# Kernel tuning notes

Hardware: AMD Instinct MI355X
Metric: run time of the kernel (lower is better)

## Reference

```python
import jax, jax.numpy as jnp
from jax import lax
import numpy as np

L = 8            # NMF rank (n_components)
NMF_ITERS = 50   # fixed multiplicative-update iterations
EPS = 1.1920929e-07  # float32 machine eps, as sklearn uses


def nmf_mu(V, key):
    """Multiplicative-update NMF (Frobenius loss), sklearn-style random init.
    V: [T, M] nonnegative. Returns W:[T,L], H:[L,M]."""
    T, M = V.shape
    kW, kH = jax.random.split(key)
    avg = jnp.sqrt(jnp.mean(V) / L)
    W0 = avg * jax.random.uniform(kW, (T, L), dtype=V.dtype)
    H0 = avg * jax.random.uniform(kH, (L, M), dtype=V.dtype)

    def step(carry, _):
        W, H = carry
        # H update: H *= (W^T V) / (W^T W H)
        H = H * (W.T @ V) / (W.T @ W @ H + EPS)
        # W update: W *= (V H^T) / (W H H^T)
        W = W * (V @ H.T) / (W @ (H @ H.T) + EPS)
        return (W, H), None

    (W, H), _ = lax.scan(step, (W0, H0), None, length=NMF_ITERS)
    return W, H


def pointwise_conv(w, x):
    # 1x1x1 Conv3d == channel mix: w [C_out, C_in], x [n, C_in, D, H, W]
    return jnp.einsum('oc,ncdhw->nodhw', w, x)


def setup_inputs() -> dict:
    key = jax.random.key(0)
    k0, k1, k2, k3, k4 = jax.random.split(key, 5)
    C = 64
    eps = jax.random.normal(k0, (1, C, 16, 64, 64), dtype=jnp.float32)
    s = 1.0 / np.sqrt(C)  # keep pre-activation variance ~1 (like torch init scale)
    w_pre = jax.random.normal(k1, (C, C), dtype=jnp.float32) * s
    b_pre = jax.random.normal(k2, (C,), dtype=jnp.float32) * s
    w_post1 = jax.random.normal(k3, (C, C), dtype=jnp.float32) * s
    w_post2 = jax.random.normal(k4, (C, C), dtype=jnp.float32) * s
    return {"eps": eps, "w_pre": w_pre, "b_pre": b_pre,
            "w_post1": w_post1, "w_post2": w_post2}


def reference(eps, w_pre, b_pre, w_post1, w_post2):
    n, t, k, a, b = eps.shape
    # xi_pre: 1x1x1 conv + bias + ReLU (ReLU guarantees nonnegative NMF input)
    Vst = jax.nn.relu(pointwise_conv(w_pre, eps) + b_pre[None, :, None, None, None])
    V = Vst.reshape(t, k * a * b)  # n == 1
    W, H = nmf_mu(V, jax.random.key(0))
    Vst_hat = (W @ H).reshape(n, t, k, a, b)
    error = jnp.linalg.norm(Vst - Vst_hat)  # torch.dist (Frobenius)
    # xi_post: conv(no bias) -> ReLU -> conv(no bias)
    y = jax.nn.relu(pointwise_conv(w_post1, Vst_hat))
    eps_hat = pointwise_conv(w_post2, y)
    return eps_hat, error
```

## Files before the change

### kernel.cpp

```cpp
#include <hip/hip_runtime.h>
#include <stdint.h>

#define JAX_PARTITIONABLE 1

constexpr int kC = 64;
constexpr int kS = 65536;
constexpr int kL = 8;
constexpr int kIters = 50;
constexpr int kBlocks = 256;
constexpr int kThreads = 512;
constexpr int kCols = 256;
constexpr int kGroups = 16;
constexpr int kEntries = 576;
constexpr float kEps = 1.1920929e-07f;

#define AGENT __HIP_MEMORY_SCOPE_AGENT

struct Ctl {
  unsigned root;  unsigned pad0[31];
  unsigned leaf[16][32];
  float mean_sum; float err_sum; float pad1[30];
  float B[3][kGroups][kEntries];
};

__device__ __forceinline__ uint2 tf2x32(unsigned k0, unsigned k1,
                                        unsigned x0, unsigned x1) {
  unsigned k2 = k0 ^ k1 ^ 0x1BD11BDAu;
  x0 += k0; x1 += k1;
#define TF_RND(r) { x0 += x1; x1 = (x1 << (r)) | (x1 >> (32 - (r))); x1 ^= x0; }
  TF_RND(13) TF_RND(15) TF_RND(26) TF_RND(6)
  x0 += k1; x1 += k2 + 1u;
  TF_RND(17) TF_RND(29) TF_RND(16) TF_RND(24)
  x0 += k2; x1 += k0 + 2u;
  TF_RND(13) TF_RND(15) TF_RND(26) TF_RND(6)
  x0 += k0; x1 += k1 + 3u;
  TF_RND(17) TF_RND(29) TF_RND(16) TF_RND(24)
  x0 += k1; x1 += k2 + 4u;
  TF_RND(13) TF_RND(15) TF_RND(26) TF_RND(6)
  x0 += k2; x1 += k0 + 5u;
#undef TF_RND
  return make_uint2(x0, x1);
}

__device__ __forceinline__ float u01(unsigned b) {
  return __uint_as_float((b >> 9) | 0x3f800000u) - 1.0f;
}

__device__ __forceinline__ void gridbar(Ctl* ctl, unsigned& round) {
  ++round;
  __syncthreads();
  if (threadIdx.x == 0) {
    const unsigned target = round * 16u;
    const unsigned leaf = blockIdx.x & 15u;
    unsigned a = __hip_atomic_fetch_add(&ctl->leaf[leaf][0], 1u,
                                        __ATOMIC_RELAXED, AGENT);
    if (a == target - 1u)
      __hip_atomic_fetch_add(&ctl->root, 1u, __ATOMIC_RELAXED, AGENT);
    while (__hip_atomic_load(&ctl->root, __ATOMIC_RELAXED, AGENT) < target)
      __builtin_amdgcn_s_sleep(1);
    __builtin_amdgcn_fence(__ATOMIC_ACQUIRE, "agent");
  }
  __syncthreads();
}

__global__ void init_ctl(unsigned* ws) {
  const unsigned n = (unsigned)(sizeof(Ctl) / 4);
  for (unsigned i = blockIdx.x * blockDim.x + threadIdx.x; i < n;
       i += gridDim.x * blockDim.x)
    ws[i] = 0u;
}

__global__ __launch_bounds__(kThreads, 2) void fsam_nmf(
    const float* __restrict__ eps, const float* __restrict__ w_pre,
    const float* __restrict__ b_pre, const float* __restrict__ w_post1,
    const float* __restrict__ w_post2, float* __restrict__ out, Ctl* ctl) {
  __shared__ __align__(16) float Vs[kC][260];
  __shared__ __align__(16) float Hs[kL][260];
  __shared__ __align__(16) float Pn[kL][260];
  __shared__ __align__(16) float Pv[4][512];
  __shared__ __align__(16) float Ph[16][64];
  __shared__ __align__(16) float Ws[kC][kL];
  __shared__ __align__(16) float WtWs[kL * kL];
  __shared__ __align__(16) float hhts[kL * kL];
  __shared__ float reds[8];

  const int tid = threadIdx.x;
  const int t = tid & 255;
  const int q = tid >> 8;
  const int obase = q * 32;
  const int s = blockIdx.x * kCols + t;
  unsigned bar_round = 0;

  float acc[32];
#pragma unroll
  for (int o = 0; o < 32; ++o) acc[o] = b_pre[obase + o];
  for (int c = 0; c < kC; ++c) {
    const float e = eps[c * kS + s];
#pragma unroll
    for (int o = 0; o < 32; ++o)
      acc[o] = fmaf(w_pre[(obase + o) * kC + c], e, acc[o]);
  }
  float lsum = 0.0f;
#pragma unroll
  for (int o = 0; o < 32; ++o) {
    acc[o] = fmaxf(acc[o], 0.0f);
    Vs[obase + o][t] = acc[o];
    lsum += acc[o];
  }
  {
    float r = lsum;
#pragma unroll
    for (int off = 32; off > 0; off >>= 1) r += __shfl_down(r, off, 64);
    if ((tid & 63) == 0) reds[tid >> 6] = r;
    __syncthreads();
    if (tid == 0) {
      float sm = 0.0f;
#pragma unroll
      for (int w = 0; w < 8; ++w) sm += reds[w];
      __hip_atomic_fetch_add(&ctl->mean_sum, sm, __ATOMIC_RELAXED, AGENT);
    }
  }
  gridbar(ctl, bar_round);
  const float avg = sqrtf(
      __hip_atomic_load(&ctl->mean_sum, __ATOMIC_RELAXED, AGENT) *
      (1.0f / (4194304.0f * 8.0f)));

#if JAX_PARTITIONABLE
  const uint2 kw = tf2x32(0u, 0u, 0u, 0u);
  const uint2 kh = tf2x32(0u, 0u, 0u, 1u);
#else
  const uint2 A0 = tf2x32(0u, 0u, 0u, 2u);
  const uint2 A1 = tf2x32(0u, 0u, 1u, 3u);
  const uint2 kw = make_uint2(A0.x, A1.x);
  const uint2 kh = make_uint2(A0.y, A1.y);
#endif

  float h[kL] = {0, 0, 0, 0, 0, 0, 0, 0};
  if (q == 0) {
#if JAX_PARTITIONABLE
#pragma unroll
    for (int l = 0; l < kL; ++l) {
      uint2 r = tf2x32(kh.x, kh.y, 0u, (unsigned)(l * kS + s));
      h[l] = avg * u01(r.x ^ r.y);
    }
#else
#pragma unroll
    for (int l = 0; l < 4; ++l) {
      unsigned i = (unsigned)(l * kS + s);
      uint2 r = tf2x32(kh.x, kh.y, i, i + 262144u);
      h[l] = avg * u01(r.x);
      h[l + 4] = avg * u01(r.y);
    }
#endif
  }
  {
#if JAX_PARTITIONABLE
    uint2 r0 = tf2x32(kw.x, kw.y, 0u, (unsigned)tid);
    (&Ws[0][0])[tid] = avg * u01(r0.x ^ r0.y);
#else
    if (tid < 256) {
      uint2 r = tf2x32(kw.x, kw.y, (unsigned)tid, (unsigned)(tid + 256));
      (&Ws[0][0])[tid] = avg * u01(r.x);
      (&Ws[0][0])[tid + 256] = avg * u01(r.y);
    }
#endif
  }
  __syncthreads();
  if (tid < kL * kL) {
    const int l = tid >> 3, j = tid & 7;
    float sum = 0.0f;
    for (int c = 0; c < kC; ++c) sum = fmaf(Ws[c][l], Ws[c][j], sum);
    WtWs[tid] = sum;
  }
  __syncthreads();

  for (int it = 0; it < kIters; ++it) {
    float num[kL] = {0, 0, 0, 0, 0, 0, 0, 0};
    for (int ci = 0; ci < 32; ++ci) {
      const int c = obase + ci;
      const float v = Vs[c][t];
      const float4 w0 = *(const float4*)&Ws[c][0];
      const float4 w1 = *(const float4*)&Ws[c][4];
      num[0] = fmaf(v, w0.x, num[0]); num[1] = fmaf(v, w0.y, num[1]);
      num[2] = fmaf(v, w0.z, num[2]); num[3] = fmaf(v, w0.w, num[3]);
      num[4] = fmaf(v, w1.x, num[4]); num[5] = fmaf(v, w1.y, num[5]);
      num[6] = fmaf(v, w1.z, num[6]); num[7] = fmaf(v, w1.w, num[7]);
    }
    if (q == 1) {
#pragma unroll
      for (int l = 0; l < kL; ++l) Pn[l][t] = num[l];
    }
    __syncthreads();
    if (q == 0) {
      float hn[kL];
#pragma unroll
      for (int l = 0; l < kL; ++l) {
        const float4 a = *(const float4*)&WtWs[l * kL];
        const float4 b = *(const float4*)&WtWs[l * kL + 4];
        float d = kEps;
        d = fmaf(a.x, h[0], d); d = fmaf(a.y, h[1], d);
        d = fmaf(a.z, h[2], d); d = fmaf(a.w, h[3], d);
        d = fmaf(b.x, h[4], d); d = fmaf(b.y, h[5], d);
        d = fmaf(b.z, h[6], d); d = fmaf(b.w, h[7], d);
        hn[l] = h[l] * (num[l] + Pn[l][t]) / d;
      }
#pragma unroll
      for (int l = 0; l < kL; ++l) { h[l] = hn[l]; Hs[l][t] = hn[l]; }
    } else if ((blockIdx.x >> 4) == 1) {
      float* nb = &ctl->B[(it + 1) % 3][blockIdx.x & 15][0];
      for (int k = t; k < kEntries; k += 256)
        __hip_atomic_store(&nb[k], 0.0f, __ATOMIC_RELAXED, AGENT);
    }
    __syncthreads();

    {
      const int range = tid >> 7;
      const int tile = tid & 127;
      const int c0 = (tile >> 2) * 2;
      const int l0 = (tile & 3) * 2;
      const int sbeg = range * 64;
      float a00 = 0, a01 = 0, a10 = 0, a11 = 0;
      for (int s4 = sbeg; s4 < sbeg + 64; s4 += 4) {
        const float4 h0 = *(const float4*)&Hs[l0][s4];
        const float4 h1 = *(const float4*)&Hs[l0 + 1][s4];
        const float4 v0 = *(const float4*)&Vs[c0][s4];
        const float4 v1 = *(const float4*)&Vs[c0 + 1][s4];
        a00 = fmaf(v0.x, h0.x, a00); a00 = fmaf(v0.y, h0.y, a00);
        a00 = fmaf(v0.z, h0.z, a00); a00 = fmaf(v0.w, h0.w, a00);
        a01 = fmaf(v0.x, h1.x, a01); a01 = fmaf(v0.y, h1.y, a01);
        a01 = fmaf(v0.z, h1.z, a01); a01 = fmaf(v0.w, h1.w, a01);
        a10 = fmaf(v1.x, h0.x, a10); a10 = fmaf(v1.y, h0.y, a10);
        a10 = fmaf(v1.z, h0.z, a10); a10 = fmaf(v1.w, h0.w, a10);
        a11 = fmaf(v1.x, h1.x, a11); a11 = fmaf(v1.y, h1.y, a11);
        a11 = fmaf(v1.z, h1.z, a11); a11 = fmaf(v1.w, h1.w, a11);
      }
      Pv[range][c0 * 8 + l0] = a00;
      Pv[range][c0 * 8 + l0 + 1] = a01;
      Pv[range][(c0 + 1) * 8 + l0] = a10;
      Pv[range][(c0 + 1) * 8 + l0 + 1] = a11;
    }
    if (tid < 256) {
      const int tile = tid >> 4, range = tid & 15;
      const int j0 = (tile >> 2) * 2, l0 = (tile & 3) * 2;
      const int sbeg = range * 16;
      float a00 = 0, a01 = 0, a10 = 0, a11 = 0;
      for (int s4 = sbeg; s4 < sbeg + 16; s4 += 4) {
        const float4 x0 = *(const float4*)&Hs[j0][s4];
        const float4 x1 = *(const float4*)&Hs[j0 + 1][s4];
        const float4 y0 = *(const float4*)&Hs[l0][s4];
        const float4 y1 = *(const float4*)&Hs[l0 + 1][s4];
        a00 = fmaf(x0.x, y0.x, a00); a00 = fmaf(x0.y, y0.y, a00);
        a00 = fmaf(x0.z, y0.z, a00); a00 = fmaf(x0.w, y0.w, a00);
        a01 = fmaf(x0.x, y1.x, a01); a01 = fmaf(x0.y, y1.y, a01);
        a01 = fmaf(x0.z, y1.z, a01); a01 = fmaf(x0.w, y1.w, a01);
        a10 = fmaf(x1.x, y0.x, a10); a10 = fmaf(x1.y, y0.y, a10);
        a10 = fmaf(x1.z, y0.z, a10); a10 = fmaf(x1.w, y0.w, a10);
        a11 = fmaf(x1.x, y1.x, a11); a11 = fmaf(x1.y, y1.y, a11);
        a11 = fmaf(x1.z, y1.z, a11); a11 = fmaf(x1.w, y1.w, a11);
      }
      Ph[range][j0 * 8 + l0] = a00;
      Ph[range][j0 * 8 + l0 + 1] = a01;
      Ph[range][(j0 + 1) * 8 + l0] = a10;
      Ph[range][(j0 + 1) * 8 + l0 + 1] = a11;
    }
    __syncthreads();

    float* Bg = &ctl->B[it % 3][blockIdx.x & 15][0];
    {
      const float v = Pv[0][tid & 511] + Pv[1][tid & 511] +
                      Pv[2][tid & 511] + Pv[3][tid & 511];
      __hip_atomic_fetch_add(&Bg[tid], v, __ATOMIC_RELAXED, AGENT);
    }
    if (tid >= 448) {
      const int e = tid - 448;
      float v = 0.0f;
#pragma unroll
      for (int r = 0; r < 16; ++r) v += Ph[r][e];
      __hip_atomic_fetch_add(&Bg[512 + e], v, __ATOMIC_RELAXED, AGENT);
    }

    gridbar(ctl, bar_round);

    const float* Bb = &ctl->B[it % 3][0][0];
    float v = 0.0f;
    {
#pragma unroll
      for (int g = 0; g < kGroups; ++g) v += Bb[g * kEntries + tid];
    }
    if (tid < kL * kL) {
      float sum = 0.0f;
#pragma unroll
      for (int g = 0; g < kGroups; ++g) sum += Bb[g * kEntries + 512 + tid];
      hhts[tid] = sum;
    }
    __syncthreads();
    float wn;
    {
      const int c0 = tid >> 3, l0 = tid & 7;
      float d = kEps;
#pragma unroll
      for (int j = 0; j < kL; ++j) d = fmaf(Ws[c0][j], hhts[j * kL + l0], d);
      wn = (&Ws[0][0])[tid] * v / d;
    }
    __syncthreads();
    (&Ws[0][0])[tid] = wn;
    __syncthreads();
    if (tid < kL * kL) {
      const int l = tid >> 3, j = tid & 7;
      float sum = 0.0f;
      for (int c = 0; c < kC; ++c) sum = fmaf(Ws[c][l], Ws[c][j], sum);
      WtWs[tid] = sum;
    }
    __syncthreads();
  }

  if (q == 1) {
#pragma unroll
    for (int l = 0; l < kL; ++l) h[l] = Hs[l][t];
  }
  float errp = 0.0f;
  for (int ci = 0; ci < 32; ++ci) {
    const int c = obase + ci;
    const float4 w0 = *(const float4*)&Ws[c][0];
    const float4 w1 = *(const float4*)&Ws[c][4];
    float tcc = 0.0f;
    tcc = fmaf(w0.x, h[0], tcc); tcc = fmaf(w0.y, h[1], tcc);
    tcc = fmaf(w0.z, h[2], tcc); tcc = fmaf(w0.w, h[3], tcc);
    tcc = fmaf(w1.x, h[4], tcc); tcc = fmaf(w1.y, h[5], tcc);
    tcc = fmaf(w1.z, h[6], tcc); tcc = fmaf(w1.w, h[7], tcc);
    const float d = Vs[c][t] - tcc;
    errp = fmaf(d, d, errp);
    Vs[c][t] = tcc;
  }
  {
    float r = errp;
#pragma unroll
    for (int off = 32; off > 0; off >>= 1) r += __shfl_down(r, off, 64);
    __syncthreads();
    if ((tid & 63) == 0) reds[tid >> 6] = r;
    __syncthreads();
    if (tid == 0) {
      float sm = 0.0f;
#pragma unroll
      for (int w = 0; w < 8; ++w) sm += reds[w];
      __hip_atomic_fetch_add(&ctl->err_sum, sm, __ATOMIC_RELAXED, AGENT);
    }
  }
  __syncthreads();
  float yacc[32];
#pragma unroll
  for (int o = 0; o < 32; ++o) yacc[o] = 0.0f;
  for (int c = 0; c < kC; ++c) {
    const float vv = Vs[c][t];
#pragma unroll
    for (int o = 0; o < 32; ++o)
      yacc[o] = fmaf(w_post1[(obase + o) * kC + c], vv, yacc[o]);
  }
  __syncthreads();
#pragma unroll
  for (int o = 0; o < 32; ++o) Vs[obase + o][t] = fmaxf(yacc[o], 0.0f);
  __syncthreads();
  float outacc[32];
#pragma unroll
  for (int o = 0; o < 32; ++o) outacc[o] = 0.0f;
  for (int c = 0; c < kC; ++c) {
    const float yv = Vs[c][t];
#pragma unroll
    for (int o = 0; o < 32; ++o)
      outacc[o] = fmaf(w_post2[(obase + o) * kC + c], yv, outacc[o]);
  }
#pragma unroll
  for (int o = 0; o < 32; ++o) out[(obase + o) * kS + s] = outacc[o];

  gridbar(ctl, bar_round);
  if (blockIdx.x == 0 && tid == 0)
    out[kC * kS] = sqrtf(__hip_atomic_load(&ctl->err_sum, __ATOMIC_RELAXED, AGENT));
}

extern "C" void kernel_launch(void* const* d_in, const int* in_sizes, int n_in,
                              void* d_out, int out_size, void* d_ws, size_t ws_size,
                              hipStream_t stream) {
  (void)in_sizes; (void)n_in; (void)out_size; (void)ws_size;
  const float* eps     = (const float*)d_in[0];
  const float* w_pre   = (const float*)d_in[1];
  const float* b_pre   = (const float*)d_in[2];
  const float* w_post1 = (const float*)d_in[3];
  const float* w_post2 = (const float*)d_in[4];
  float* out = (float*)d_out;
  Ctl* ctl = (Ctl*)d_ws;

  init_ctl<<<64, 256, 0, stream>>>((unsigned*)d_ws);
  fsam_nmf<<<kBlocks, kThreads, 0, stream>>>(eps, w_pre, b_pre, w_post1,
                                             w_post2, out, ctl);
}
```

Before: 741.3 us.

## Restructure NMF kernel with transposed V tile, register-resident V, fewer reduction groups

Reworks the per-block NMF loop. V now lives in registers as two columns per thread, with a transposed shared-memory copy used for the V·H^T reduction. The numerator partial sums are split across four channel groups, and W^T W is computed in parallel chunks inside the loop instead of by 64 threads serially. The number of global reduction groups drops from 16 to 4. The goal is to cut shared-memory traffic and serial per-iteration work, at the cost of more atomic contention per group and more register pressure.

```diff
diff --git a/kernel.cpp b/kernel.cpp
--- a/kernel.cpp
+++ b/kernel.cpp
@@ -10,8 +10,11 @@
 constexpr int kBlocks = 256;
 constexpr int kThreads = 512;
 constexpr int kCols = 256;
-constexpr int kGroups = 16;
+constexpr int kGroups = 4;
 constexpr int kEntries = 576;
+constexpr int kHP = 260;
+constexpr int kVP = 68;
+constexpr int kNP = 258;
 constexpr float kEps = 1.1920929e-07f;
 
 #define AGENT __HIP_MEMORY_SCOPE_AGENT
@@ -50,12 +53,12 @@
   ++round;
   __syncthreads();
   if (threadIdx.x == 0) {
-    const unsigned target = round * 16u;
     const unsigned leaf = blockIdx.x & 15u;
     unsigned a = __hip_atomic_fetch_add(&ctl->leaf[leaf][0], 1u,
                                         __ATOMIC_RELAXED, AGENT);
-    if (a == target - 1u)
+    if (a == round * 16u - 1u)
       __hip_atomic_fetch_add(&ctl->root, 1u, __ATOMIC_RELAXED, AGENT);
+    const unsigned target = round * 16u;
     while (__hip_atomic_load(&ctl->root, __ATOMIC_RELAXED, AGENT) < target)
       __builtin_amdgcn_s_sleep(1);
     __builtin_amdgcn_fence(__ATOMIC_ACQUIRE, "agent");
@@ -74,38 +77,49 @@
     const float* __restrict__ eps, const float* __restrict__ w_pre,
     const float* __restrict__ b_pre, const float* __restrict__ w_post1,
     const float* __restrict__ w_post2, float* __restrict__ out, Ctl* ctl) {
-  __shared__ __align__(16) float Vs[kC][260];
-  __shared__ __align__(16) float Hs[kL][260];
-  __shared__ __align__(16) float Pn[kL][260];
-  __shared__ __align__(16) float Pv[4][512];
+  __shared__ __align__(16) float Vt[kCols][kVP];
+  __shared__ __align__(16) float Hs[kL][kHP];
+  __shared__ __align__(16) float Pn[4][kL][kNP];
+  __shared__ __align__(16) float Pv[8][512];
   __shared__ __align__(16) float Ph[16][64];
+  __shared__ __align__(16) float Pw[8][64];
   __shared__ __align__(16) float Ws[kC][kL];
-  __shared__ __align__(16) float WtWs[kL * kL];
-  __shared__ __align__(16) float hhts[kL * kL];
+  __shared__ __align__(16) float WtWs[64];
+  __shared__ __align__(16) float hhts[64];
   __shared__ float reds[8];
 
   const int tid = threadIdx.x;
-  const int t = tid & 255;
-  const int q = tid >> 8;
-  const int obase = q * 32;
-  const int s = blockIdx.x * kCols + t;
+  const int g = tid >> 7;
+  const int p = tid & 127;
+  const int obase = g * 16;
+  const int sb = blockIdx.x * kCols;
   unsigned bar_round = 0;
 
-  float acc[32];
-#pragma unroll
-  for (int o = 0; o < 32; ++o) acc[o] = b_pre[obase + o];
+  float vreg[2][16];
+#pragma unroll
+  for (int o = 0; o < 16; ++o) { vreg[0][o] = b_pre[obase + o]; vreg[1][o] = vreg[0][o]; }
   for (int c = 0; c < kC; ++c) {
-    const float e = eps[c * kS + s];
-#pragma unroll
-    for (int o = 0; o < 32; ++o)
-      acc[o] = fmaf(w_pre[(obase + o) * kC + c], e, acc[o]);
+    const float2 e2 = *(const float2*)(eps + (size_t)c * kS + sb + 2 * p);
+#pragma unroll
+    for (int o = 0; o < 16; ++o) {
+      const float w = w_pre[(obase + o) * kC + c];
+      vreg[0][o] = fmaf(w, e2.x, vreg[0][o]);
+      vreg[1][o] = fmaf(w, e2.y, vreg[1][o]);
+    }
   }
   float lsum = 0.0f;
 #pragma unroll
-  for (int o = 0; o < 32; ++o) {
-    acc[o] = fmaxf(acc[o], 0.0f);
-    Vs[obase + o][t] = acc[o];
-    lsum += acc[o];
+  for (int col = 0; col < 2; ++col) {
+#pragma unroll
+    for (int o = 0; o < 16; ++o) {
+      vreg[col][o] = fmaxf(vreg[col][o], 0.0f);
+      lsum += vreg[col][o];
+    }
+#pragma unroll
+    for (int k = 0; k < 4; ++k)
+      *(float4*)&Vt[2 * p + col][obase + 4 * k] =
+          make_float4(vreg[col][4 * k], vreg[col][4 * k + 1],
+                      vreg[col][4 * k + 2], vreg[col][4 * k + 3]);
   }
   {
     float r = lsum;
@@ -134,22 +148,21 @@
   const uint2 kw = make_uint2(A0.x, A1.x);
   const uint2 kh = make_uint2(A0.y, A1.y);
 #endif
-
-  float h[kL] = {0, 0, 0, 0, 0, 0, 0, 0};
-  if (q == 0) {
+  if (tid < 256) {
+    const int s = sb + tid;
 #if JAX_PARTITIONABLE
 #pragma unroll
     for (int l = 0; l < kL; ++l) {
       uint2 r = tf2x32(kh.x, kh.y, 0u, (unsigned)(l * kS + s));
-      h[l] = avg * u01(r.x ^ r.y);
+      Hs[l][tid] = avg * u01(r.x ^ r.y);
     }
 #else
 #pragma unroll
     for (int l = 0; l < 4; ++l) {
       unsigned i = (unsigned)(l * kS + s);
       uint2 r = tf2x32(kh.x, kh.y, i, i + 262144u);
-      h[l] = avg * u01(r.x);
-      h[l + 4] = avg * u01(r.y);
+      Hs[l][tid] = avg * u01(r.x);
+      Hs[l + 4][tid] = avg * u01(r.y);
     }
 #endif
   }
@@ -166,85 +179,74 @@
 #endif
   }
   __syncthreads();
-  if (tid < kL * kL) {
-    const int l = tid >> 3, j = tid & 7;
-    float sum = 0.0f;
-    for (int c = 0; c < kC; ++c) sum = fmaf(Ws[c][l], Ws[c][j], sum);
-    WtWs[tid] = sum;
-  }
-  __syncthreads();
 
   for (int it = 0; it < kIters; ++it) {
-    float num[kL] = {0, 0, 0, 0, 0, 0, 0, 0};
-    for (int ci = 0; ci < 32; ++ci) {
-      const int c = obase + ci;
-      const float v = Vs[c][t];
-      const float4 w0 = *(const float4*)&Ws[c][0];
-      const float4 w1 = *(const float4*)&Ws[c][4];
-      num[0] = fmaf(v, w0.x, num[0]); num[1] = fmaf(v, w0.y, num[1]);
-      num[2] = fmaf(v, w0.z, num[2]); num[3] = fmaf(v, w0.w, num[3]);
-      num[4] = fmaf(v, w1.x, num[4]); num[5] = fmaf(v, w1.y, num[5]);
-      num[6] = fmaf(v, w1.z, num[6]); num[7] = fmaf(v, w1.w, num[7]);
-    }
-    if (q == 1) {
-#pragma unroll
-      for (int l = 0; l < kL; ++l) Pn[l][t] = num[l];
-    }
-    __syncthreads();
-    if (q == 0) {
-      float hn[kL];
-#pragma unroll
-      for (int l = 0; l < kL; ++l) {
-        const float4 a = *(const float4*)&WtWs[l * kL];
-        const float4 b = *(const float4*)&WtWs[l * kL + 4];
-        float d = kEps;
-        d = fmaf(a.x, h[0], d); d = fmaf(a.y, h[1], d);
-        d = fmaf(a.z, h[2], d); d = fmaf(a.w, h[3], d);
-        d = fmaf(b.x, h[4], d); d = fmaf(b.y, h[5], d);
-        d = fmaf(b.z, h[6], d); d = fmaf(b.w, h[7], d);
-        hn[l] = h[l] * (num[l] + Pn[l][t]) / d;
+    {
+      const int e = tid & 63, chunk = tid >> 6, cb = chunk * 8;
+      const int l = e >> 3, j = e & 7;
+      float s = 0.0f;
+#pragma unroll
+      for (int cc = 0; cc < 8; ++cc)
+        s = fmaf(Ws[cb + cc][l], Ws[cb + cc][j], s);
+      Pw[chunk][e] = s;
+    }
+    {
+      float num[2][kL] = {};
+#pragma unroll
+      for (int ci = 0; ci < 16; ++ci) {
+        const int c = obase + ci;
+        const float4 w0 = *(const float4*)&Ws[c][0];
+        const float4 w1 = *(const float4*)&Ws[c][4];
+        const float v0 = vreg[0][ci], v1 = vreg[1][ci];
+        num[0][0] = fmaf(v0, w0.x, num[0][0]); num[0][1] = fmaf(v0, w0.y, num[0][1]);
+        num[0][2] = fmaf(v0, w0.z, num[0][2]); num[0][3] = fmaf(v0, w0.w, num[0][3]);
+        num[0][4] = fmaf(v0, w1.x, num[0][4]); num[0][5] = fmaf(v0, w1.y, num[0][5]);
+        num[0][6] = fmaf(v0, w1.z, num[0][6]); num[0][7] = fmaf(v0, w1.w, num[0][7]);
+        num[1][0] = fmaf(v1, w0.x, num[1][0]); num[1][1] = fmaf(v1, w0.y, num[1][1]);
+        num[1][2] = fmaf(v1, w0.z, num[1][2]); num[1][3] = fmaf(v1, w0.w, num[1][3]);
+        num[1][4] = fmaf(v1, w1.x, num[1][4]); num[1][5] = fmaf(v1, w1.y, num[1][5]);
+        num[1][6] = fmaf(v1, w1.z, num[1][6]); num[1][7] = fmaf(v1, w1.w, num[1][7]);
       }
 #pragma unroll
-      for (int l = 0; l < kL; ++l) { h[l] = hn[l]; Hs[l][t] = hn[l]; }
-    } else if ((blockIdx.x >> 4) == 1) {
-      float* nb = &ctl->B[(it + 1) % 3][blockIdx.x & 15][0];
-      for (int k = t; k < kEntries; k += 256)
-        __hip_atomic_store(&nb[k], 0.0f, __ATOMIC_RELAXED, AGENT);
-    }
-    __syncthreads();
-
-    {
-      const int range = tid >> 7;
-      const int tile = tid & 127;
-      const int c0 = (tile >> 2) * 2;
-      const int l0 = (tile & 3) * 2;
-      const int sbeg = range * 64;
+      for (int l = 0; l < kL; ++l)
+        *(float2*)&Pn[g][l][2 * p] = make_float2(num[0][l], num[1][l]);
+    }
+    __syncthreads();
+    const int col = tid & 255, lh = tid >> 8;
+    float h[kL], nm[4];
+#pragma unroll
+    for (int l = 0; l < kL; ++l) h[l] = Hs[l][col];
+#pragma unroll
+    for (int k = 0; k < 4; ++k) {
+      const int l = lh * 4 + k;
+      nm[k] = Pn[0][l][col] + Pn[1][l][col] + Pn[2][l][col] + Pn[3][l][col];
+    }
+    if (tid < 64) {
+      float s = 0.0f;
+#pragma unroll
+      for (int r = 0; r < 8; ++r) s += Pw[r][tid];
+      WtWs[tid] = s;
+    }
+    __syncthreads();
+#pragma unroll
+    for (int k = 0; k < 4; ++k) {
+      const int l = lh * 4 + k;
+      const float4 a = *(const float4*)&WtWs[l * kL];
+      const float4 b = *(const float4*)&WtWs[l * kL + 4];
+      float d = kEps;
+      d = fmaf(a.x, h[0], d); d = fmaf(a.y, h[1], d);
+      d = fmaf(a.z, h[2], d); d = fmaf(a.w, h[3], d);
+      d = fmaf(b.x, h[4], d); d = fmaf(b.y, h[5], d);
+      d = fmaf(b.z, h[6], d); d = fmaf(b.w, h[7], d);
+      Hs[l][col] = h[l] * nm[k] / d;
+    }
+    __syncthreads();
+    if (tid < 256) {
+      const int tle = tid & 15, rng = tid >> 4;
+      const int j0 = (tle >> 2) * 2, l0 = (tle & 3) * 2;
+      const int s0 = rng * 16;
       float a00 = 0, a01 = 0, a10 = 0, a11 = 0;
-      for (int s4 = sbeg; s4 < sbeg + 64; s4 += 4) {
-        const float4 h0 = *(const float4*)&Hs[l0][s4];
-        const float4 h1 = *(const float4*)&Hs[l0 + 1][s4];
-        const float4 v0 = *(const float4*)&Vs[c0][s4];
-        const float4 v1 = *(const float4*)&Vs[c0 + 1][s4];
-        a00 = fmaf(v0.x, h0.x, a00); a00 = fmaf(v0.y, h0.y, a00);
-        a00 = fmaf(v0.z, h0.z, a00); a00 = fmaf(v0.w, h0.w, a00);
-        a01 = fmaf(v0.x, h1.x, a01); a01 = fmaf(v0.y, h1.y, a01);
-        a01 = fmaf(v0.z, h1.z, a01); a01 = fmaf(v0.w, h1.w, a01);
-        a10 = fmaf(v1.x, h0.x, a10); a10 = fmaf(v1.y, h0.y, a10);
-        a10 = fmaf(v1.z, h0.z, a10); a10 = fmaf(v1.w, h0.w, a10);
-        a11 = fmaf(v1.x, h1.x, a11); a11 = fmaf(v1.y, h1.y, a11);
-        a11 = fmaf(v1.z, h1.z, a11); a11 = fmaf(v1.w, h1.w, a11);
-      }
-      Pv[range][c0 * 8 + l0] = a00;
-      Pv[range][c0 * 8 + l0 + 1] = a01;
-      Pv[range][(c0 + 1) * 8 + l0] = a10;
-      Pv[range][(c0 + 1) * 8 + l0 + 1] = a11;
-    }
-    if (tid < 256) {
-      const int tile = tid >> 4, range = tid & 15;
-      const int j0 = (tile >> 2) * 2, l0 = (tile & 3) * 2;
-      const int sbeg = range * 16;
-      float a00 = 0, a01 = 0, a10 = 0, a11 = 0;
-      for (int s4 = sbeg; s4 < sbeg + 16; s4 += 4) {
+      for (int s4 = s0; s4 < s0 + 16; s4 += 4) {
         const float4 x0 = *(const float4*)&Hs[j0][s4];
         const float4 x1 = *(const float4*)&Hs[j0 + 1][s4];
         const float4 y0 = *(const float4*)&Hs[l0][s4];
@@ -258,80 +260,127 @@
         a11 = fmaf(x1.x, y1.x, a11); a11 = fmaf(x1.y, y1.y, a11);
         a11 = fmaf(x1.z, y1.z, a11); a11 = fmaf(x1.w, y1.w, a11);
       }
-      Ph[range][j0 * 8 + l0] = a00;
-      Ph[range][j0 * 8 + l0 + 1] = a01;
-      Ph[range][(j0 + 1) * 8 + l0] = a10;
-      Ph[range][(j0 + 1) * 8 + l0 + 1] = a11;
-    }
-    __syncthreads();
-
-    float* Bg = &ctl->B[it % 3][blockIdx.x & 15][0];
+      Ph[rng][j0 * 8 + l0] = a00;
+      Ph[rng][j0 * 8 + l0 + 1] = a01;
+      Ph[rng][(j0 + 1) * 8 + l0] = a10;
+      Ph[rng][(j0 + 1) * 8 + l0 + 1] = a11;
+    }
     {
-      const float v = Pv[0][tid & 511] + Pv[1][tid & 511] +
-                      Pv[2][tid & 511] + Pv[3][tid & 511];
+      const int tile = tid & 63, rng = tid >> 6;
+      const int cq = tile & 15, lp = tile >> 4;
+      const int cb = cq * 4, lb = lp * 2;
+      float acc[4][2] = {};
+      for (int s4 = rng * 32; s4 < rng * 32 + 32; s4 += 4) {
+        const float4 h0 = *(const float4*)&Hs[lb][s4];
+        const float4 h1 = *(const float4*)&Hs[lb + 1][s4];
+        const float4 va = *(const float4*)&Vt[s4][cb];
+        const float4 vb = *(const float4*)&Vt[s4 + 1][cb];
+        const float4 vc = *(const float4*)&Vt[s4 + 2][cb];
+        const float4 vd = *(const float4*)&Vt[s4 + 3][cb];
+        acc[0][0] = fmaf(va.x, h0.x, acc[0][0]); acc[0][1] = fmaf(va.x, h1.x, acc[0][1]);
+        acc[1][0] = fmaf(va.y, h0.x, acc[1][0]); acc[1][1] = fmaf(va.y, h1.x, acc[1][1]);
+        acc[2][0] = fmaf(va.z, h0.x, acc[2][0]); acc[2][1] = fmaf(va.z, h1.x, acc[2][1]);
+        acc[3][0] = fmaf(va.w, h0.x, acc[3][0]); acc[3][1] = fmaf(va.w, h1.x, acc[3][1]);
+        acc[0][0] = fmaf(vb.x, h0.y, acc[0][0]); acc[0][1] = fmaf(vb.x, h1.y, acc[0][1]);
+        acc[1][0] = fmaf(vb.y, h0.y, acc[1][0]); acc[1][1] = fmaf(vb.y, h1.y, acc[1][1]);
+        acc[2][0] = fmaf(vb.z, h0.y, acc[2][0]); acc[2][1] = fmaf(vb.z, h1.y, acc[2][1]);
+        acc[3][0] = fmaf(vb.w, h0.y, acc[3][0]); acc[3][1] = fmaf(vb.w, h1.y, acc[3][1]);
+        acc[0][0] = fmaf(vc.x, h0.z, acc[0][0]); acc[0][1] = fmaf(vc.x, h1.z, acc[0][1]);
+        acc[1][0] = fmaf(vc.y, h0.z, acc[1][0]); acc[1][1] = fmaf(vc.y, h1.z, acc[1][1]);
+        acc[2][0] = fmaf(vc.z, h0.z, acc[2][0]); acc[2][1] = fmaf(vc.z, h1.z, acc[2][1]);
+        acc[3][0] = fmaf(vc.w, h0.z, acc[3][0]); acc[3][1] = fmaf(vc.w, h1.z, acc[3][1]);
+        acc[0][0] = fmaf(vd.x, h0.w, acc[0][0]); acc[0][1] = fmaf(vd.x, h1.w, acc[0][1]);
+        acc[1][0] = fmaf(vd.y, h0.w, acc[1][0]); acc[1][1] = fmaf(vd.y, h1.w, acc[1][1]);
+        acc[2][0] = fmaf(vd.z, h0.w, acc[2][0]); acc[2][1] = fmaf(vd.z, h1.w, acc[2][1]);
+        acc[3][0] = fmaf(vd.w, h0.w, acc[3][0]); acc[3][1] = fmaf(vd.w, h1.w, acc[3][1]);
+      }
+#pragma unroll
+      for (int j = 0; j < 4; ++j)
+        *(float2*)&Pv[rng][cq * 32 + lp * 8 + j * 2] =
+            make_float2(acc[j][0], acc[j][1]);
+    }
+    __syncthreads();
+    float* Bg = &ctl->B[it % 3][blockIdx.x & 3][0];
+    {
+      const int c = tid >> 3, l = tid & 7;
+      const int slot = (c >> 2) * 32 + (l >> 1) * 8 + (c & 3) * 2 + (l & 1);
+      float v = 0.0f;
+#pragma unroll
+      for (int r = 0; r < 8; ++r) v += Pv[r][slot];
       __hip_atomic_fetch_add(&Bg[tid], v, __ATOMIC_RELAXED, AGENT);
     }
-    if (tid >= 448) {
-      const int e = tid - 448;
+    if (tid < 64) {
       float v = 0.0f;
 #pragma unroll
-      for (int r = 0; r < 16; ++r) v += Ph[r][e];
-      __hip_atomic_fetch_add(&Bg[512 + e], v, __ATOMIC_RELAXED, AGENT);
+      for (int r = 0; r < 16; ++r) v += Ph[r][tid];
+      __hip_atomic_fetch_add(&Bg[512 + tid], v, __ATOMIC_RELAXED, AGENT);
+    }
+    if ((blockIdx.x >> 2) == 4) {
+      float* nb = &ctl->B[(it + 1) % 3][blockIdx.x & 3][0];
+      __hip_atomic_store(&nb[tid], 0.0f, __ATOMIC_RELAXED, AGENT);
+      if (tid < 64)
+        __hip_atomic_store(&nb[512 + tid], 0.0f, __ATOMIC_RELAXED, AGENT);
     }
 
     gridbar(ctl, bar_round);
 
     const float* Bb = &ctl->B[it % 3][0][0];
-    float v = 0.0f;
-    {
-#pragma unroll
-      for (int g = 0; g < kGroups; ++g) v += Bb[g * kEntries + tid];
-    }
-    if (tid < kL * kL) {
-      float sum = 0.0f;
-#pragma unroll
-      for (int g = 0; g < kGroups; ++g) sum += Bb[g * kEntries + 512 + tid];
-      hhts[tid] = sum;
+    float v = Bb[tid] + Bb[kEntries + tid] + Bb[2 * kEntries + tid] +
+              Bb[3 * kEntries + tid];
+    if (tid < 64) {
+      hhts[tid] = Bb[512 + tid] + Bb[kEntries + 512 + tid] +
+                  Bb[2 * kEntries + 512 + tid] + Bb[3 * kEntries + 512 + tid];
     }
     __syncthreads();
     float wn;
     {
       const int c0 = tid >> 3, l0 = tid & 7;
+      const float4 w0 = *(const float4*)&Ws[c0][0];
+      const float4 w1 = *(const float4*)&Ws[c0][4];
       float d = kEps;
-#pragma unroll
-      for (int j = 0; j < kL; ++j) d = fmaf(Ws[c0][j], hhts[j * kL + l0], d);
+      d = fmaf(w0.x, hhts[l0], d);      d = fmaf(w0.y, hhts[8 + l0], d);
+      d = fmaf(w0.z, hhts[16 + l0], d); d = fmaf(w0.w, hhts[24 + l0], d);
+      d = fmaf(w1.x, hhts[32 + l0], d); d = fmaf(w1.y, hhts[40 + l0], d);
+      d = fmaf(w1.z, hhts[48 + l0], d); d = fmaf(w1.w, hhts[56 + l0], d);
       wn = (&Ws[0][0])[tid] * v / d;
     }
     __syncthreads();
     (&Ws[0][0])[tid] = wn;
     __syncthreads();
-    if (tid < kL * kL) {
-      const int l = tid >> 3, j = tid & 7;
-      float sum = 0.0f;
-      for (int c = 0; c < kC; ++c) sum = fmaf(Ws[c][l], Ws[c][j], sum);
-      WtWs[tid] = sum;
-    }
-    __syncthreads();
-  }
-
-  if (q == 1) {
-#pragma unroll
-    for (int l = 0; l < kL; ++l) h[l] = Hs[l][t];
+  }
+
+  float h2[2][kL];
+#pragma unroll
+  for (int l = 0; l < kL; ++l) {
+    const float2 t2 = *(const float2*)&Hs[l][2 * p];
+    h2[0][l] = t2.x; h2[1][l] = t2.y;
   }
   float errp = 0.0f;
-  for (int ci = 0; ci < 32; ++ci) {
+  float vh[2][16];
+#pragma unroll
+  for (int ci = 0; ci < 16; ++ci) {
     const int c = obase + ci;
     const float4 w0 = *(const float4*)&Ws[c][0];
     const float4 w1 = *(const float4*)&Ws[c][4];
-    float tcc = 0.0f;
-    tcc = fmaf(w0.x, h[0], tcc); tcc = fmaf(w0.y, h[1], tcc);
-    tcc = fmaf(w0.z, h[2], tcc); tcc = fmaf(w0.w, h[3], tcc);
-    tcc = fmaf(w1.x, h[4], tcc); tcc = fmaf(w1.y, h[5], tcc);
-    tcc = fmaf(w1.z, h[6], tcc); tcc = fmaf(w1.w, h[7], tcc);
-    const float d = Vs[c][t] - tcc;
-    errp = fmaf(d, d, errp);
-    Vs[c][t] = tcc;
-  }
+#pragma unroll
+    for (int colx = 0; colx < 2; ++colx) {
+      float t = 0.0f;
+      t = fmaf(w0.x, h2[colx][0], t); t = fmaf(w0.y, h2[colx][1], t);
+      t = fmaf(w0.z, h2[colx][2], t); t = fmaf(w0.w, h2[colx][3], t);
+      t = fmaf(w1.x, h2[colx][4], t); t = fmaf(w1.y, h2[colx][5], t);
+      t = fmaf(w1.z, h2[colx][6], t); t = fmaf(w1.w, h2[colx][7], t);
+      vh[colx][ci] = t;
+      const float d = vreg[colx][ci] - t;
+      errp = fmaf(d, d, errp);
+    }
+  }
+#pragma unroll
+  for (int colx = 0; colx < 2; ++colx)
+#pragma unroll
+    for (int k = 0; k < 4; ++k)
+      *(float4*)&Vt[2 * p + colx][obase + 4 * k] =
+          make_float4(vh[colx][4 * k], vh[colx][4 * k + 1],
+                      vh[colx][4 * k + 2], vh[colx][4 * k + 3]);
   {
     float r = errp;
 #pragma unroll
@@ -347,34 +396,50 @@
     }
   }
   __syncthreads();
-  float yacc[32];
-#pragma unroll
-  for (int o = 0; o < 32; ++o) yacc[o] = 0.0f;
-  for (int c = 0; c < kC; ++c) {
-    const float vv = Vs[c][t];
-#pragma unroll
-    for (int o = 0; o < 32; ++o)
-      yacc[o] = fmaf(w_post1[(obase + o) * kC + c], vv, yacc[o]);
-  }
-  __syncthreads();
-#pragma unroll
-  for (int o = 0; o < 32; ++o) Vs[obase + o][t] = fmaxf(yacc[o], 0.0f);
-  __syncthreads();
-  float outacc[32];
-#pragma unroll
-  for (int o = 0; o < 32; ++o) outacc[o] = 0.0f;
-  for (int c = 0; c < kC; ++c) {
-    const float yv = Vs[c][t];
-#pragma unroll
-    for (int o = 0; o < 32; ++o)
-      outacc[o] = fmaf(w_post2[(obase + o) * kC + c], yv, outacc[o]);
-  }
-#pragma unroll
-  for (int o = 0; o < 32; ++o) out[(obase + o) * kS + s] = outacc[o];
+  float ya[2][16] = {};
+  for (int cb = 0; cb < 16; ++cb) {
+    const float4 v0 = *(const float4*)&Vt[2 * p][cb * 4];
+    const float4 v1 = *(const float4*)&Vt[2 * p + 1][cb * 4];
+#pragma unroll
+    for (int o = 0; o < 16; ++o) {
+      const float* wr = &w_post1[(obase + o) * kC + cb * 4];
+      ya[0][o] = fmaf(wr[0], v0.x, ya[0][o]); ya[1][o] = fmaf(wr[0], v1.x, ya[1][o]);
+      ya[0][o] = fmaf(wr[1], v0.y, ya[0][o]); ya[1][o] = fmaf(wr[1], v1.y, ya[1][o]);
+      ya[0][o] = fmaf(wr[2], v0.z, ya[0][o]); ya[1][o] = fmaf(wr[2], v1.z, ya[1][o]);
+      ya[0][o] = fmaf(wr[3], v0.w, ya[0][o]); ya[1][o] = fmaf(wr[3], v1.w, ya[1][o]);
+    }
+  }
+  __syncthreads();
+#pragma unroll
+  for (int colx = 0; colx < 2; ++colx)
+#pragma unroll
+    for (int k = 0; k < 4; ++k)
+      *(float4*)&Vt[2 * p + colx][obase + 4 * k] =
+          make_float4(fmaxf(ya[colx][4 * k], 0.0f), fmaxf(ya[colx][4 * k + 1], 0.0f),
+                      fmaxf(ya[colx][4 * k + 2], 0.0f), fmaxf(ya[colx][4 * k + 3], 0.0f));
+  __syncthreads();
+  float oa[2][16] = {};
+  for (int cb = 0; cb < 16; ++cb) {
+    const float4 v0 = *(const float4*)&Vt[2 * p][cb * 4];
+    const float4 v1 = *(const float4*)&Vt[2 * p + 1][cb * 4];
+#pragma unroll
+    for (int o = 0; o < 16; ++o) {
+      const float* wr = &w_post2[(obase + o) * kC + cb * 4];
+      oa[0][o] = fmaf(wr[0], v0.x, oa[0][o]); oa[1][o] = fmaf(wr[0], v1.x, oa[1][o]);
+      oa[0][o] = fmaf(wr[1], v0.y, oa[0][o]); oa[1][o] = fmaf(wr[1], v1.y, oa[1][o]);
+      oa[0][o] = fmaf(wr[2], v0.z, oa[0][o]); oa[1][o] = fmaf(wr[2], v1.z, oa[1][o]);
+      oa[0][o] = fmaf(wr[3], v0.w, oa[0][o]); oa[1][o] = fmaf(wr[3], v1.w, oa[1][o]);
+    }
+  }
+#pragma unroll
+  for (int o = 0; o < 16; ++o)
+    *(float2*)&out[(size_t)(obase + o) * kS + sb + 2 * p] =
+        make_float2(oa[0][o], oa[1][o]);
 
   gridbar(ctl, bar_round);
   if (blockIdx.x == 0 && tid == 0)
-    out[kC * kS] = sqrtf(__hip_atomic_load(&ctl->err_sum, __ATOMIC_RELAXED, AGENT));
+    out[(size_t)kC * kS] =
+        sqrtf(__hip_atomic_load(&ctl->err_sum, __ATOMIC_RELAXED, AGENT));
 }
 
 extern "C" void kernel_launch(void* const* d_in, const int* in_sizes, int n_in,
```

Measured after the change: 647.0 us. 1.15x faster.
